# Optimization experiments

Hardware: AMD Instinct MI355X
Metric: run time of the kernel (lower is better)

Reference implementation:

```python
import jax, jax.numpy as jnp
import numpy as np

N_NODES = 50000
N_EDGES = 800000
IN_CH = 128
HID_CH = 256
N_GRAPHS = 500


def setup_inputs() -> dict:
    key = jax.random.key(0)
    k = jax.random.split(key, 8)
    x = jax.random.normal(k[0], (N_NODES, IN_CH), dtype=jnp.float32)
    edge_index = jax.random.randint(k[1], (2, N_EDGES), 0, N_NODES, dtype=jnp.int32)
    batch = jnp.sort(jax.random.randint(k[2], (N_NODES,), 0, N_GRAPHS, dtype=jnp.int32))
    # GCNConv weights (glorot-ish scaling) and zero biases, Linear fc is unused in forward
    W1 = jax.random.normal(k[3], (IN_CH, HID_CH), dtype=jnp.float32) / np.sqrt(IN_CH)
    b1 = jnp.zeros((HID_CH,), dtype=jnp.float32)
    W2 = jax.random.normal(k[4], (HID_CH, HID_CH), dtype=jnp.float32) / np.sqrt(HID_CH)
    b2 = jnp.zeros((HID_CH,), dtype=jnp.float32)
    return {"x": x, "W1": W1, "b1": b1, "W2": W2, "b2": b2,
            "edge_index": edge_index, "batch": batch}


def _gcn_conv(x, W, b, src, dst, norm, n_nodes):
    # x' = scatter_add_dst( norm_e * (x @ W)[src] ) + b   (self-loops already in src/dst)
    xw = x @ W                              # [N, H]
    msg = xw[src] * norm[:, None]           # [E+N, H]
    out = jax.ops.segment_sum(msg, dst, num_segments=n_nodes)
    return out + b


def reference(x, W1, b1, W2, b2, edge_index, batch):
    n = x.shape[0]
    # add self-loops (PyG GCNConv default)
    loop = jnp.arange(n, dtype=edge_index.dtype)
    src = jnp.concatenate([edge_index[0], loop])
    dst = jnp.concatenate([edge_index[1], loop])
    # symmetric normalization D^{-1/2} (A+I) D^{-1/2}; deg from dst counts
    deg = jax.ops.segment_sum(jnp.ones_like(dst, dtype=x.dtype), dst, num_segments=n)
    dis = jnp.where(deg > 0, jax.lax.rsqrt(deg), 0.0)
    norm = dis[src] * dis[dst]              # [E+N]

    h = jax.nn.relu(_gcn_conv(x, W1, b1, src, dst, norm, n))
    h = jax.nn.relu(_gcn_conv(h, W2, b2, src, dst, norm, n))

    # global_mean_pool over batch ids
    sums = jax.ops.segment_sum(h, batch, num_segments=N_GRAPHS)
    cnts = jax.ops.segment_sum(jnp.ones((n,), dtype=h.dtype), batch, num_segments=N_GRAPHS)
    return sums / jnp.maximum(cnts, 1.0)[:, None]
```

## Files before the change

kernel.cpp:

```cpp
#include <hip/hip_runtime.h>

#define HID 256
#define SLOTS 32
#define OVCAP 16384
#define CS 16
typedef unsigned short ushort_t;
typedef unsigned int uint_t;
typedef __attribute__((ext_vector_type(8))) short short8;
typedef __attribute__((ext_vector_type(4))) float f32x4;
typedef __attribute__((ext_vector_type(4))) unsigned short us4;
typedef __attribute__((ext_vector_type(8))) unsigned short us8;

__device__ __forceinline__ ushort_t f2b(float f) {
    uint_t u = __float_as_uint(f);
    u = u + 0x7fffu + ((u >> 16) & 1u);
    return (ushort_t)(u >> 16);
}

__global__ __launch_bounds__(256) void k_countfill(const int* __restrict__ src,
                                                   const int* __restrict__ dst,
                                                   int* __restrict__ cnt,
                                                   int* __restrict__ csr2,
                                                   int* __restrict__ ovn,
                                                   int2* __restrict__ ov, int E) {
    int i = blockIdx.x * 256 + threadIdx.x;
    if (i >= E) return;
    int d = dst[i], s = src[i];
    int c = atomicAdd(&cnt[d * CS], 1);
    if (c < SLOTS) {
        csr2[d * SLOTS + c] = s;
    } else {
        int p = atomicAdd(ovn, 1);
        if (p < OVCAP) ov[p] = make_int2(d, s);
    }
}

__global__ __launch_bounds__(256) void k_castprep(const float* __restrict__ x,
                                                  const int* __restrict__ cnt,
                                                  ushort_t* __restrict__ xg,
                                                  const float* __restrict__ W1,
                                                  ushort_t* __restrict__ Wt1,
                                                  const float* __restrict__ W2,
                                                  ushort_t* __restrict__ Wt2,
                                                  int n, int rshift, int p1b, int p2b) {
    int bid = blockIdx.x;
    if (bid < p1b + p2b) {
        const float* W = (bid < p1b) ? W1 : W2;
        ushort_t* Wt = (bid < p1b) ? Wt1 : Wt2;
        int kg = (bid < p1b) ? bid : bid - p1b;
        int c = threadIdx.x;
        float v = W[(size_t)kg * HID + c];
        int p = kg >> 6;
        int k = kg & 63;
        int byte_ = c * 128 + k * 2;
        int slot = byte_ >> 4;
        int sw = (slot & ~7) | ((slot ^ c) & 7);
        size_t dst_byte = (size_t)p * 32768 + ((size_t)sw << 4) + (byte_ & 15);
        Wt[dst_byte >> 1] = f2b(v);
        return;
    }
    int i = (bid - p1b - p2b) * 256 + threadIdx.x;
    int total8 = n << rshift;
    if (i >= total8) return;
    int r = i >> rshift;
    int j = i & ((1 << rshift) - 1);
    float dv = rsqrtf((float)(cnt[r * CS] + 1));
    const float4* p = (const float4*)(x + (size_t)i * 8);
    float4 v0 = p[0], v1 = p[1];
    us8 o;
    o[0] = f2b(v0.x * dv); o[1] = f2b(v0.y * dv); o[2] = f2b(v0.z * dv); o[3] = f2b(v0.w * dv);
    o[4] = f2b(v1.x * dv); o[5] = f2b(v1.y * dv); o[6] = f2b(v1.z * dv); o[7] = f2b(v1.w * dv);
    size_t dst = (size_t)(j >> 2) * ((size_t)n * 32) + (size_t)r * 32 + (size_t)(j & 3) * 8;
    *(us8*)(xg + dst) = o;
}

#define ACC8(r)                                                            \
    a0 += __uint_as_float((r).x << 16); a1 += __uint_as_float((r).x & 0xffff0000u); \
    a2 += __uint_as_float((r).y << 16); a3 += __uint_as_float((r).y & 0xffff0000u); \
    a4 += __uint_as_float((r).z << 16); a5 += __uint_as_float((r).z & 0xffff0000u); \
    a6 += __uint_as_float((r).w << 16); a7 += __uint_as_float((r).w & 0xffff0000u);

template <int NG>
__global__ __launch_bounds__(256) void k_agg_g(const ushort_t* __restrict__ Yg,
                                               ushort_t* __restrict__ Z,
                                               const int* __restrict__ cnt,
                                               const int* __restrict__ csr2,
                                               const int* __restrict__ ovn,
                                               const int2* __restrict__ ov, int n) {
    const int LOG = (NG == 8) ? 3 : 2;
    const int g = blockIdx.x & (NG - 1);
    const int chunk = blockIdx.x >> LOG;
    const int q = threadIdx.x >> 4;
    const int l16 = threadIdx.x & 15;
    const int v = chunk * 16 + q;
    if (v >= n) return;
    const int par = l16 >> 2;
    const int sub = l16 & 3;
    const uint4* Yb = (const uint4*)(Yg + (size_t)g * ((size_t)n * 32));
    uint4 self;
    if (par == 0) self = Yb[(uint_t)v * 4u + sub];
    const int deg = cnt[v * CS];
    const int lim = min(deg, SLOTS);
    const int* row = csr2 + v * SLOTS;
    float a0 = 0.f, a1 = 0.f, a2 = 0.f, a3 = 0.f, a4 = 0.f, a5 = 0.f, a6 = 0.f, a7 = 0.f;
    int e = par;
    while (e + 4 < lim) {
        int s0 = row[e], s1 = row[e + 4];
        uint4 r0 = Yb[(uint_t)s0 * 4u + sub];
        uint4 r1 = Yb[(uint_t)s1 * 4u + sub];
        ACC8(r0); ACC8(r1);
        e += 8;
    }
    if (e < lim) {
        int s0 = row[e];
        uint4 r0 = Yb[(uint_t)s0 * 4u + sub];
        ACC8(r0);
    }
    if (deg > SLOTS) {
        int m = min(*ovn, OVCAP);
        for (int i2 = par; i2 < m; i2 += 4) {
            int2 p = ov[i2];
            if (p.x == v) { uint4 r = Yb[(uint_t)p.y * 4u + sub]; ACC8(r); }
        }
    }
    a0 += __shfl_xor(a0, 4, 64); a1 += __shfl_xor(a1, 4, 64);
    a2 += __shfl_xor(a2, 4, 64); a3 += __shfl_xor(a3, 4, 64);
    a4 += __shfl_xor(a4, 4, 64); a5 += __shfl_xor(a5, 4, 64);
    a6 += __shfl_xor(a6, 4, 64); a7 += __shfl_xor(a7, 4, 64);
    a0 += __shfl_xor(a0, 8, 64); a1 += __shfl_xor(a1, 8, 64);
    a2 += __shfl_xor(a2, 8, 64); a3 += __shfl_xor(a3, 8, 64);
    a4 += __shfl_xor(a4, 8, 64); a5 += __shfl_xor(a5, 8, 64);
    a6 += __shfl_xor(a6, 8, 64); a7 += __shfl_xor(a7, 8, 64);
    if (par == 0) {
        ACC8(self);
        float dv = rsqrtf((float)(deg + 1));
        us8 o;
        o[0] = f2b(a0 * dv); o[1] = f2b(a1 * dv); o[2] = f2b(a2 * dv); o[3] = f2b(a3 * dv);
        o[4] = f2b(a4 * dv); o[5] = f2b(a5 * dv); o[6] = f2b(a6 * dv); o[7] = f2b(a7 * dv);
        *(us8*)(Z + (size_t)v * (NG * 32) + g * 32 + sub * 8) = o;
    }
}

template <int K, bool SCALE, bool OUTG>
__global__ __launch_bounds__(512) void k_gemm_mfma(const ushort_t* __restrict__ A,
                                                   const ushort_t* __restrict__ Wt,
                                                   const int* __restrict__ cnt,
                                                   const float* __restrict__ bias,
                                                   ushort_t* __restrict__ Yout, int M) {
    __shared__ char lds[49152];
    char* As = lds;
    char* Bs = lds + 16384;
    const int tid = threadIdx.x;
    const int lane = tid & 63;
    const int w = tid >> 6;
    const int wm = w & 1;
    const int wn = w >> 1;
    const int row0 = blockIdx.x * 128;

    f32x4 acc[4][4];
#pragma unroll
    for (int i = 0; i < 4; ++i)
#pragma unroll
        for (int j = 0; j < 4; ++j) acc[i][j] = (f32x4){0.f, 0.f, 0.f, 0.f};

    for (int k0 = 0; k0 < K; k0 += 64) {
#pragma unroll
        for (int q = 0; q < 2; ++q) {
            int s = q * 512 + tid;
            int r = s >> 3;
            int kseg = (s & 7) ^ (r & 7);
            int row = row0 + r;
            if (row >= M) row = 0;
            const ushort_t* g = A + (size_t)row * K + k0 + kseg * 8;
            __builtin_amdgcn_global_load_lds((const uint_t*)g,
                                             (uint_t*)(As + q * 8192 + w * 1024), 16, 0, 0);
        }
        const ushort_t* gp = Wt + (size_t)(k0 >> 6) * (256 * 64);
#pragma unroll
        for (int q = 0; q < 4; ++q) {
            int s = q * 512 + tid;
            __builtin_amdgcn_global_load_lds((const uint_t*)(gp + (size_t)s * 8),
                                             (uint_t*)(Bs + q * 8192 + w * 1024), 16, 0, 0);
        }
        __syncthreads();
#pragma unroll
        for (int k32 = 0; k32 < 2; ++k32) {
            const int ksl = k32 * 4 + (lane >> 4);
            short8 wf[4], xf[4];
#pragma unroll
            for (int nn = 0; nn < 4; ++nn) {
                int col = wn * 64 + nn * 16 + (lane & 15);
                int slot = col * 8 + (ksl ^ (col & 7));
                wf[nn] = *(const short8*)(Bs + slot * 16);
            }
#pragma unroll
            for (int m = 0; m < 4; ++m) {
                int row = wm * 64 + m * 16 + (lane & 15);
                int slot = row * 8 + (ksl ^ (row & 7));
                xf[m] = *(const short8*)(As + slot * 16);
            }
#pragma unroll
            for (int nn = 0; nn < 4; ++nn)
#pragma unroll
                for (int m = 0; m < 4; ++m)
                    acc[nn][m] = __builtin_amdgcn_mfma_f32_16x16x32_bf16(wf[nn], xf[m],
                                                                         acc[nn][m], 0, 0, 0);
        }
        __syncthreads();
    }
    const int m_lo = lane & 15, c_hi = lane >> 4;
#pragma unroll
    for (int m = 0; m < 4; ++m) {
        int row = row0 + wm * 64 + m * 16 + m_lo;
        if (row < M) {
            float dv = SCALE ? rsqrtf((float)(cnt[row * CS] + 1)) : 1.f;
#pragma unroll
            for (int nn = 0; nn < 4; ++nn) {
                int c0 = wn * 64 + nn * 16 + c_hi * 4;
                float4 bb = *(const float4*)(bias + c0);
                us4 o;
                o[0] = f2b(fmaxf(acc[nn][m][0] + bb.x, 0.f) * dv);
                o[1] = f2b(fmaxf(acc[nn][m][1] + bb.y, 0.f) * dv);
                o[2] = f2b(fmaxf(acc[nn][m][2] + bb.z, 0.f) * dv);
                o[3] = f2b(fmaxf(acc[nn][m][3] + bb.w, 0.f) * dv);
                size_t dst = OUTG
                    ? ((size_t)(c0 >> 5) * ((size_t)M * 32) + (size_t)row * 32 + (c0 & 31))
                    : ((size_t)row * HID + c0);
                *(us4*)(Yout + dst) = o;
            }
        }
    }
}

__global__ __launch_bounds__(256) void k_pool2(const ushort_t* __restrict__ H,
                                               const int* __restrict__ batch,
                                               float* __restrict__ out, int n) {
    __shared__ int se[2];
    int g = blockIdx.x;
    if (threadIdx.x < 2) {
        int tgt = g + (int)threadIdx.x;
        int lo = 0, hi = n;
        while (lo < hi) { int mid = (lo + hi) >> 1; if (batch[mid] < tgt) lo = mid + 1; else hi = mid; }
        se[threadIdx.x] = lo;
    }
    __syncthreads();
    int s = se[0], e = se[1];
    int c = threadIdx.x;
    float sum = 0.f;
    for (int i = s; i < e; ++i)
        sum += __uint_as_float(((uint_t)H[(size_t)i * HID + c]) << 16);
    out[(size_t)g * HID + c] = sum / (float)max(e - s, 1);
}

extern "C" void kernel_launch(void* const* d_in, const int* in_sizes, int n_in,
                              void* d_out, int out_size, void* d_ws, size_t ws_size,
                              hipStream_t stream) {
    const float* x = (const float*)d_in[0];
    const float* W1 = (const float*)d_in[1];
    const float* b1 = (const float*)d_in[2];
    const float* W2 = (const float*)d_in[3];
    const float* b2 = (const float*)d_in[4];
    const int* ei = (const int*)d_in[5];
    const int* batch = (const int*)d_in[6];
    float* out = (float*)d_out;

    const int N = in_sizes[6];
    const int E = in_sizes[5] / 2;
    const int K1 = in_sizes[0] / N;
    const int G = out_size / HID;
    (void)n_in; (void)ws_size;

    char* w = (char*)d_ws;
    int* cnt = (int*)(w + 0);
    int* ovn = (int*)(w + 3200000);
    int2* ov = (int2*)(w + 3200064);
    int* csr2 = (int*)(w + 3331136);
    ushort_t* Wt1 = (ushort_t*)(w + 9731136);
    ushort_t* Wt2 = (ushort_t*)(w + 9796672);
    ushort_t* Xg = (ushort_t*)(w + 9927744);
    ushort_t* Z1 = (ushort_t*)(w + 22727744);
    ushort_t* H1g = (ushort_t*)(w + 35527744);
    ushort_t* Z2 = (ushort_t*)(w + 9927744);
    ushort_t* H2 = (ushort_t*)(w + 35527744);

    hipMemsetAsync(cnt, 0, 3200064, stream);

    const int eb = (E + 255) / 256;
    k_countfill<<<eb, 256, 0, stream>>>(ei, ei + E, cnt, csr2, ovn, ov, E);

    int rshift = 31 - __builtin_clz((unsigned)(K1 / 8));
    int castb = (N * K1 / 8 + 255) / 256;
    k_castprep<<<K1 + HID + castb, 256, 0, stream>>>(x, cnt, Xg, W1, Wt1, W2, Wt2,
                                                     N, rshift, K1, HID);

    int gblk = (N + 127) / 128;
    const int chunks = (N + 15) / 16;
    k_agg_g<4><<<4 * chunks, 256, 0, stream>>>(Xg, Z1, cnt, csr2, ovn, ov, N);
    k_gemm_mfma<128, true, true><<<gblk, 512, 0, stream>>>(Z1, Wt1, cnt, b1, H1g, N);
    k_agg_g<8><<<8 * chunks, 256, 0, stream>>>(H1g, Z2, cnt, csr2, ovn, ov, N);
    k_gemm_mfma<256, false, false><<<gblk, 512, 0, stream>>>(Z2, Wt2, cnt, b2, H2, N);

    k_pool2<<<G, 256, 0, stream>>>(H2, batch, out, N);
}
```

Baseline: 227.0 us.

## Fuse CSR build with cast prep, move src-degree scaling into aggregation

Merges the edge count/fill kernel and the bf16 cast/weight-swizzle kernel into one launch, which is possible because the cast no longer needs degrees. The source-side D^-1/2 scaling moves from the cast into the first aggregation through a precomputed dis array gathered per neighbor. The aggregation loop is restructured so each of four lanes-groups loads 8 neighbor indices as two int4 and issues all 8 row gathers at once to raise memory-level parallelism. This adds a small k_dis kernel and extra per-edge dis loads in layer 1, and issues predicated loads even for low-degree nodes.

```diff
diff --git a/kernel.cpp b/kernel.cpp
--- a/kernel.cpp
+++ b/kernel.cpp
@@ -17,37 +17,37 @@
     return (ushort_t)(u >> 16);
 }
 
-__global__ __launch_bounds__(256) void k_countfill(const int* __restrict__ src,
-                                                   const int* __restrict__ dst,
-                                                   int* __restrict__ cnt,
-                                                   int* __restrict__ csr2,
-                                                   int* __restrict__ ovn,
-                                                   int2* __restrict__ ov, int E) {
-    int i = blockIdx.x * 256 + threadIdx.x;
-    if (i >= E) return;
-    int d = dst[i], s = src[i];
-    int c = atomicAdd(&cnt[d * CS], 1);
-    if (c < SLOTS) {
-        csr2[d * SLOTS + c] = s;
-    } else {
-        int p = atomicAdd(ovn, 1);
-        if (p < OVCAP) ov[p] = make_int2(d, s);
-    }
-}
-
-__global__ __launch_bounds__(256) void k_castprep(const float* __restrict__ x,
-                                                  const int* __restrict__ cnt,
-                                                  ushort_t* __restrict__ xg,
-                                                  const float* __restrict__ W1,
-                                                  ushort_t* __restrict__ Wt1,
-                                                  const float* __restrict__ W2,
-                                                  ushort_t* __restrict__ Wt2,
-                                                  int n, int rshift, int p1b, int p2b) {
+__global__ __launch_bounds__(256) void k_mega(const int* __restrict__ src,
+                                              const int* __restrict__ dstp,
+                                              int* __restrict__ cnt,
+                                              int* __restrict__ csr2,
+                                              int* __restrict__ ovn,
+                                              int2* __restrict__ ov, int E,
+                                              const float* __restrict__ x,
+                                              ushort_t* __restrict__ xg,
+                                              const float* __restrict__ W1,
+                                              ushort_t* __restrict__ Wt1,
+                                              const float* __restrict__ W2,
+                                              ushort_t* __restrict__ Wt2,
+                                              int n, int rshift, int eb, int p1b, int p2b) {
     int bid = blockIdx.x;
-    if (bid < p1b + p2b) {
-        const float* W = (bid < p1b) ? W1 : W2;
-        ushort_t* Wt = (bid < p1b) ? Wt1 : Wt2;
-        int kg = (bid < p1b) ? bid : bid - p1b;
+    if (bid < eb) {
+        int i = bid * 256 + threadIdx.x;
+        if (i >= E) return;
+        int d = dstp[i], s = src[i];
+        int c = atomicAdd(&cnt[d * CS], 1);
+        if (c < SLOTS) {
+            csr2[d * SLOTS + c] = s;
+        } else {
+            int p = atomicAdd(ovn, 1);
+            if (p < OVCAP) ov[p] = make_int2(d, s);
+        }
+        return;
+    }
+    if (bid < eb + p1b + p2b) {
+        const float* W = (bid < eb + p1b) ? W1 : W2;
+        ushort_t* Wt = (bid < eb + p1b) ? Wt1 : Wt2;
+        int kg = (bid < eb + p1b) ? (bid - eb) : (bid - eb - p1b);
         int c = threadIdx.x;
         float v = W[(size_t)kg * HID + c];
         int p = kg >> 6;
@@ -59,19 +59,24 @@
         Wt[dst_byte >> 1] = f2b(v);
         return;
     }
-    int i = (bid - p1b - p2b) * 256 + threadIdx.x;
+    int i = (bid - eb - p1b - p2b) * 256 + threadIdx.x;
     int total8 = n << rshift;
     if (i >= total8) return;
     int r = i >> rshift;
     int j = i & ((1 << rshift) - 1);
-    float dv = rsqrtf((float)(cnt[r * CS] + 1));
     const float4* p = (const float4*)(x + (size_t)i * 8);
     float4 v0 = p[0], v1 = p[1];
     us8 o;
-    o[0] = f2b(v0.x * dv); o[1] = f2b(v0.y * dv); o[2] = f2b(v0.z * dv); o[3] = f2b(v0.w * dv);
-    o[4] = f2b(v1.x * dv); o[5] = f2b(v1.y * dv); o[6] = f2b(v1.z * dv); o[7] = f2b(v1.w * dv);
+    o[0] = f2b(v0.x); o[1] = f2b(v0.y); o[2] = f2b(v0.z); o[3] = f2b(v0.w);
+    o[4] = f2b(v1.x); o[5] = f2b(v1.y); o[6] = f2b(v1.z); o[7] = f2b(v1.w);
     size_t dst = (size_t)(j >> 2) * ((size_t)n * 32) + (size_t)r * 32 + (size_t)(j & 3) * 8;
     *(us8*)(xg + dst) = o;
+}
+
+__global__ __launch_bounds__(256) void k_dis(const int* __restrict__ cnt,
+                                             float* __restrict__ dis, int n) {
+    int v = blockIdx.x * 256 + threadIdx.x;
+    if (v < n) dis[v] = rsqrtf((float)(cnt[v * CS] + 1));
 }
 
 #define ACC8(r)                                                            \
@@ -80,13 +85,32 @@
     a4 += __uint_as_float((r).z << 16); a5 += __uint_as_float((r).z & 0xffff0000u); \
     a6 += __uint_as_float((r).w << 16); a7 += __uint_as_float((r).w & 0xffff0000u);
 
-template <int NG>
+#define ACC8F(r, d)                                                        \
+    a0 = fmaf(__uint_as_float((r).x << 16), d, a0);                        \
+    a1 = fmaf(__uint_as_float((r).x & 0xffff0000u), d, a1);                \
+    a2 = fmaf(__uint_as_float((r).y << 16), d, a2);                        \
+    a3 = fmaf(__uint_as_float((r).y & 0xffff0000u), d, a3);                \
+    a4 = fmaf(__uint_as_float((r).z << 16), d, a4);                        \
+    a5 = fmaf(__uint_as_float((r).z & 0xffff0000u), d, a5);                \
+    a6 = fmaf(__uint_as_float((r).w << 16), d, a6);                        \
+    a7 = fmaf(__uint_as_float((r).w & 0xffff0000u), d, a7);
+
+#define GATH(J, IX)                                                        \
+    uint4 r##J = make_uint4(0u, 0u, 0u, 0u);                               \
+    float d##J = 0.f;                                                      \
+    if (base + J < lim) {                                                  \
+        r##J = Yb[(uint_t)(IX) * 4u + sub];                                \
+        if (ED) d##J = dis[IX];                                            \
+    }
+
+template <int NG, bool ED>
 __global__ __launch_bounds__(256) void k_agg_g(const ushort_t* __restrict__ Yg,
                                                ushort_t* __restrict__ Z,
                                                const int* __restrict__ cnt,
                                                const int* __restrict__ csr2,
                                                const int* __restrict__ ovn,
-                                               const int2* __restrict__ ov, int n) {
+                                               const int2* __restrict__ ov,
+                                               const float* __restrict__ dis, int n) {
     const int LOG = (NG == 8) ? 3 : 2;
     const int g = blockIdx.x & (NG - 1);
     const int chunk = blockIdx.x >> LOG;
@@ -97,30 +121,33 @@
     const int par = l16 >> 2;
     const int sub = l16 & 3;
     const uint4* Yb = (const uint4*)(Yg + (size_t)g * ((size_t)n * 32));
-    uint4 self;
-    if (par == 0) self = Yb[(uint_t)v * 4u + sub];
+    uint4 self = Yb[(uint_t)v * 4u + sub];
     const int deg = cnt[v * CS];
     const int lim = min(deg, SLOTS);
-    const int* row = csr2 + v * SLOTS;
+    const int base = par * 8;
+    const int4* rp = (const int4*)(csr2 + v * SLOTS + base);
     float a0 = 0.f, a1 = 0.f, a2 = 0.f, a3 = 0.f, a4 = 0.f, a5 = 0.f, a6 = 0.f, a7 = 0.f;
-    int e = par;
-    while (e + 4 < lim) {
-        int s0 = row[e], s1 = row[e + 4];
-        uint4 r0 = Yb[(uint_t)s0 * 4u + sub];
-        uint4 r1 = Yb[(uint_t)s1 * 4u + sub];
-        ACC8(r0); ACC8(r1);
-        e += 8;
-    }
-    if (e < lim) {
-        int s0 = row[e];
-        uint4 r0 = Yb[(uint_t)s0 * 4u + sub];
-        ACC8(r0);
+    if (base < lim) {
+        int4 iA = rp[0], iB = rp[1];
+        GATH(0, iA.x); GATH(1, iA.y); GATH(2, iA.z); GATH(3, iA.w);
+        GATH(4, iB.x); GATH(5, iB.y); GATH(6, iB.z); GATH(7, iB.w);
+        if (ED) {
+            ACC8F(r0, d0); ACC8F(r1, d1); ACC8F(r2, d2); ACC8F(r3, d3);
+            ACC8F(r4, d4); ACC8F(r5, d5); ACC8F(r6, d6); ACC8F(r7, d7);
+        } else {
+            ACC8(r0); ACC8(r1); ACC8(r2); ACC8(r3);
+            ACC8(r4); ACC8(r5); ACC8(r6); ACC8(r7);
+        }
     }
     if (deg > SLOTS) {
         int m = min(*ovn, OVCAP);
         for (int i2 = par; i2 < m; i2 += 4) {
             int2 p = ov[i2];
-            if (p.x == v) { uint4 r = Yb[(uint_t)p.y * 4u + sub]; ACC8(r); }
+            if (p.x == v) {
+                uint4 r = Yb[(uint_t)p.y * 4u + sub];
+                if (ED) { float dd = dis[p.y]; ACC8F(r, dd); }
+                else { ACC8(r); }
+            }
         }
     }
     a0 += __shfl_xor(a0, 4, 64); a1 += __shfl_xor(a1, 4, 64);
@@ -132,8 +159,13 @@
     a4 += __shfl_xor(a4, 8, 64); a5 += __shfl_xor(a5, 8, 64);
     a6 += __shfl_xor(a6, 8, 64); a7 += __shfl_xor(a7, 8, 64);
     if (par == 0) {
-        ACC8(self);
-        float dv = rsqrtf((float)(deg + 1));
+        float dv = dis[v];
+        if (ED) {
+            float sd = dv;
+            ACC8F(self, sd);
+        } else {
+            ACC8(self);
+        }
         us8 o;
         o[0] = f2b(a0 * dv); o[1] = f2b(a1 * dv); o[2] = f2b(a2 * dv); o[3] = f2b(a3 * dv);
         o[4] = f2b(a4 * dv); o[5] = f2b(a5 * dv); o[6] = f2b(a6 * dv); o[7] = f2b(a7 * dv);
@@ -275,29 +307,30 @@
     int* ovn = (int*)(w + 3200000);
     int2* ov = (int2*)(w + 3200064);
     int* csr2 = (int*)(w + 3331136);
-    ushort_t* Wt1 = (ushort_t*)(w + 9731136);
-    ushort_t* Wt2 = (ushort_t*)(w + 9796672);
-    ushort_t* Xg = (ushort_t*)(w + 9927744);
-    ushort_t* Z1 = (ushort_t*)(w + 22727744);
-    ushort_t* H1g = (ushort_t*)(w + 35527744);
-    ushort_t* Z2 = (ushort_t*)(w + 9927744);
-    ushort_t* H2 = (ushort_t*)(w + 35527744);
+    float* dis = (float*)(w + 9731136);
+    ushort_t* Wt1 = (ushort_t*)(w + 9931136);
+    ushort_t* Wt2 = (ushort_t*)(w + 9996672);
+    ushort_t* Xg = (ushort_t*)(w + 10127744);
+    ushort_t* Z1 = (ushort_t*)(w + 22927744);
+    ushort_t* H1g = (ushort_t*)(w + 35727744);
+    ushort_t* Z2 = (ushort_t*)(w + 10127744);
+    ushort_t* H2 = (ushort_t*)(w + 35727744);
 
     hipMemsetAsync(cnt, 0, 3200064, stream);
 
     const int eb = (E + 255) / 256;
-    k_countfill<<<eb, 256, 0, stream>>>(ei, ei + E, cnt, csr2, ovn, ov, E);
-
     int rshift = 31 - __builtin_clz((unsigned)(K1 / 8));
     int castb = (N * K1 / 8 + 255) / 256;
-    k_castprep<<<K1 + HID + castb, 256, 0, stream>>>(x, cnt, Xg, W1, Wt1, W2, Wt2,
-                                                     N, rshift, K1, HID);
+    k_mega<<<eb + K1 + HID + castb, 256, 0, stream>>>(ei, ei + E, cnt, csr2, ovn, ov, E,
+                                                      x, Xg, W1, Wt1, W2, Wt2,
+                                                      N, rshift, eb, K1, HID);
+    k_dis<<<(N + 255) / 256, 256, 0, stream>>>(cnt, dis, N);
 
     int gblk = (N + 127) / 128;
     const int chunks = (N + 15) / 16;
-    k_agg_g<4><<<4 * chunks, 256, 0, stream>>>(Xg, Z1, cnt, csr2, ovn, ov, N);
+    k_agg_g<4, true><<<4 * chunks, 256, 0, stream>>>(Xg, Z1, cnt, csr2, ovn, ov, dis, N);
     k_gemm_mfma<128, true, true><<<gblk, 512, 0, stream>>>(Z1, Wt1, cnt, b1, H1g, N);
-    k_agg_g<8><<<8 * chunks, 256, 0, stream>>>(H1g, Z2, cnt, csr2, ovn, ov, N);
+    k_agg_g<8, false><<<8 * chunks, 256, 0, stream>>>(H1g, Z2, cnt, csr2, ovn, ov, dis, N);
     k_gemm_mfma<256, false, false><<<gblk, 512, 0, stream>>>(Z2, Wt2, cnt, b2, H2, N);
 
     k_pool2<<<G, 256, 0, stream>>>(H2, batch, out, N);
```

Result: slower. 246.2 us (+8.4%).
